# Optimization experiments

Measured on AMD Instinct MI355X. Metric: run time of the kernel, lower is better.

Reference implementation:

```python
import jax, jax.numpy as jnp
import numpy as np

HEAD_SIZE = 128  # hidden_size 2048 / 16 heads; used only as softmax scale in this module


def setup_inputs() -> dict:
    key = jax.random.key(0)
    ks = jax.random.split(key, 4)
    B, S, H = 2, 4096, 2048
    hidden_states = jax.random.normal(ks[0], (B, S, H), dtype=jnp.float32)
    attention_mask = jnp.zeros((B, 1, S), dtype=jnp.float32)  # additive mask, broadcasts onto [B,S,S]
    s = 1.0 / np.sqrt(H)
    Wq = jax.random.normal(ks[1], (H, H), dtype=jnp.float32) * s
    Wk = jax.random.normal(ks[2], (H, H), dtype=jnp.float32) * s
    Wv = jax.random.normal(ks[3], (H, H), dtype=jnp.float32) * s
    bq = jnp.zeros((H,), dtype=jnp.float32)
    bk = jnp.zeros((H,), dtype=jnp.float32)
    bv = jnp.zeros((H,), dtype=jnp.float32)
    return {"hidden_states": hidden_states, "attention_mask": attention_mask,
            "Wq": Wq, "bq": bq, "Wk": Wk, "bk": bk, "Wv": Wv, "bv": bv}


def reference(hidden_states, attention_mask, Wq, bq, Wk, bk, Wv, bv):
    # Self-attention: cross_hidden_states defaults to hidden_states.
    q = jnp.einsum('bsh,oh->bso', hidden_states, Wq) + bq  # [B,S,H]
    k = jnp.einsum('bsh,oh->bso', hidden_states, Wk) + bk
    v = jnp.einsum('bsh,oh->bso', hidden_states, Wv) + bv
    # Note: module never splits heads, so scores are a single [B,S,S] matrix
    scores = jnp.einsum('bqh,bkh->bqk', q, k) / jnp.sqrt(jnp.asarray(HEAD_SIZE, q.dtype))
    scores = scores + attention_mask  # additive mask, broadcast
    probs = jax.nn.softmax(scores, axis=-1)  # dropout p=0 -> identity
    context = jnp.einsum('bqk,bkh->bqh', probs, v)  # [B,S,H]
    return context
```

## Files before the change

### kernel.cpp

```cpp
#include <hip/hip_runtime.h>

typedef _Float16 f16;
typedef _Float16 f16x8 __attribute__((ext_vector_type(8)));
typedef _Float16 f16x4 __attribute__((ext_vector_type(4)));
typedef float    f32x16 __attribute__((ext_vector_type(16)));

#define GLD16(g, l)                                                            \
  __builtin_amdgcn_global_load_lds(                                            \
      (const __attribute__((address_space(1))) void*)(g),                      \
      (__attribute__((address_space(3))) void*)(l), 16, 0, 0)

static constexpr int S = 4096, H = 2048, B = 2;

__global__ __launch_bounds__(256) void cast_all(
    const float* __restrict__ hs, const float* __restrict__ w0,
    const float* __restrict__ w1, const float* __restrict__ w2,
    f16* __restrict__ hs_h, f16* __restrict__ w_h) {
  const int hsN4 = B * S * H / 4;
  const int wN4  = H * H / 4;
  int i = blockIdx.x * 256 + threadIdx.x;
  float4 f;
  if (i < hsN4) {
    f = reinterpret_cast<const float4*>(hs)[i];
    f16x4 h = {(f16)f.x, (f16)f.y, (f16)f.z, (f16)f.w};
    reinterpret_cast<f16x4*>(hs_h)[i] = h;
  } else {
    int j = i - hsN4;
    int seg = j / wN4, off = j - seg * wN4;
    const float* src = seg == 0 ? w0 : (seg == 1 ? w1 : w2);
    f = reinterpret_cast<const float4*>(src)[off];
    f16x4 h = {(f16)f.x, (f16)f.y, (f16)f.z, (f16)f.w};
    reinterpret_cast<f16x4*>(w_h)[j] = h;
  }
}

template <int MODE>
__global__ __launch_bounds__(256) void gemm_tn(
    const f16* __restrict__ A, const f16* __restrict__ Bm,
    void* __restrict__ C0, void* __restrict__ C1, void* __restrict__ C2,
    const float* __restrict__ x0, const float* __restrict__ x1,
    const float* __restrict__ x2, float scale, int K, int lda, int ldb) {
  __shared__ __attribute__((aligned(16))) char smem[32768];
  f16* sA = (f16*)smem;
  f16* sB = (f16*)(smem + 16384);

  const int tileM = blockIdx.y * 128;
  const int tileN = blockIdx.x * 128;

  const int tid  = threadIdx.x;
  const int wave = tid >> 6, lane = tid & 63;
  const int wm = (wave >> 1) * 64, wn = (wave & 1) * 64;
  const int l31 = lane & 31, khalf = lane >> 5;

  f32x16 acc[2][2] = {};

  size_t rowA = tileM, rowB = tileN;
  if (MODE == 2) rowB = (size_t)(tileM >> 12) * S + tileN;
  if (MODE == 3) rowB = (size_t)(tileM >> 12) * H + tileN;
  const f16* gA = A + rowA * lda;
  const f16* gB = Bm + rowB * ldb;

  size_t aoff[4], boff[4];
  int ldsoff[4];
#pragma unroll
  for (int j = 0; j < 4; ++j) {
    int id = j * 256 + tid;
    int r = id >> 3, cs = (id & 7) ^ (r & 7) ^ ((r & 16) >> 2);
    aoff[j] = (size_t)r * lda + cs * 8;
    boff[j] = (size_t)r * ldb + cs * 8;
    ldsoff[j] = id * 8;
  }

  const int rsw = (l31 & 7) ^ ((l31 & 16) >> 2);

  for (int k0 = 0; k0 < K; k0 += 64) {
#pragma unroll
    for (int j = 0; j < 4; ++j) {
      GLD16(gA + aoff[j] + k0, &sA[ldsoff[j]]);
      GLD16(gB + boff[j] + k0, &sB[ldsoff[j]]);
    }
    __syncthreads();
#pragma unroll
    for (int c = 0; c < 4; ++c) {
      f16x8 af[2], bf[2];
      const int pos = ((c * 2 + khalf) ^ rsw) * 8;
#pragma unroll
      for (int x = 0; x < 2; ++x)
        af[x] = *reinterpret_cast<const f16x8*>(&sA[(wm + x * 32 + l31) * 64 + pos]);
#pragma unroll
      for (int y = 0; y < 2; ++y)
        bf[y] = *reinterpret_cast<const f16x8*>(&sB[(wn + y * 32 + l31) * 64 + pos]);
#pragma unroll
      for (int x = 0; x < 2; ++x)
#pragma unroll
        for (int y = 0; y < 2; ++y)
          acc[x][y] = __builtin_amdgcn_mfma_f32_32x32x16_f16(af[x], bf[y], acc[x][y], 0, 0, 0);
    }
    __syncthreads();
  }

  if (MODE == 0 && (tileN >> 11) == 2) {
    const int nn0 = tileN - 2 * H;
    const int b = tileM >> 12, s0 = tileM & (S - 1);
    f16* sT = (f16*)smem;
#pragma unroll
    for (int p = 0; p < 2; ++p) {
      if ((wn >> 6) == p) {
#pragma unroll
        for (int x = 0; x < 2; ++x)
#pragma unroll
          for (int y = 0; y < 2; ++y) {
            int scol = y * 32 + l31;
            float bias = x2[nn0 + p * 64 + scol];
#pragma unroll
            for (int g = 0; g < 4; ++g) {
              int row = wm + x * 32 + g * 8 + khalf * 4;
              f16x4 h4 = {(f16)(acc[x][y][g * 4 + 0] + bias),
                          (f16)(acc[x][y][g * 4 + 1] + bias),
                          (f16)(acc[x][y][g * 4 + 2] + bias),
                          (f16)(acc[x][y][g * 4 + 3] + bias)};
              *reinterpret_cast<f16x4*>(&sT[scol * 136 + row]) = h4;
            }
          }
      }
      __syncthreads();
      {
        int c = tid >> 2, hh = tid & 3;
        const f16* src = &sT[c * 136 + hh * 32];
        f16* dst = (f16*)C2 + (size_t)b * H * S + (size_t)(nn0 + p * 64 + c) * S +
                   s0 + hh * 32;
#pragma unroll
        for (int j = 0; j < 4; ++j)
          reinterpret_cast<f16x8*>(dst)[j] = reinterpret_cast<const f16x8*>(src)[j];
      }
      __syncthreads();
    }
    return;
  }

#pragma unroll
  for (int x = 0; x < 2; ++x)
#pragma unroll
    for (int y = 0; y < 2; ++y)
#pragma unroll
      for (int r = 0; r < 16; ++r) {
        int m = tileM + wm + x * 32 + (r & 3) + 8 * (r >> 2) + 4 * khalf;
        int n = tileN + wn + y * 32 + l31;
        float v = acc[x][y][r];
        if (MODE == 0) {
          int seg = n >> 11, nn = n & 2047;
          if (seg == 0) {
            ((f16*)C0)[(size_t)m * H + nn] = (f16)(v + x0[nn]);
          } else {
            ((f16*)C1)[(size_t)m * H + nn] = (f16)(v + x1[nn]);
          }
        } else if (MODE == 2) {
          int b = m >> 12;
          ((f16*)C0)[(size_t)m * S + n] = (f16)(v * scale + x0[(size_t)b * S + n]);
        } else {
          ((float*)C0)[(size_t)m * H + n] = v;
        }
      }
}

__global__ __launch_bounds__(256) void softmax_f16(f16* __restrict__ sc) {
  const int tid = threadIdx.x;
  f16* rp = sc + (size_t)blockIdx.x * S;
  f16x8 h[2];
#pragma unroll
  for (int j = 0; j < 2; ++j) h[j] = reinterpret_cast<f16x8*>(rp)[tid + j * 256];

  float v[16];
#pragma unroll
  for (int j = 0; j < 2; ++j)
#pragma unroll
    for (int e = 0; e < 8; ++e) v[j * 8 + e] = (float)h[j][e];

  float m = -1e30f;
#pragma unroll
  for (int e = 0; e < 16; ++e) m = fmaxf(m, v[e]);
#pragma unroll
  for (int off = 32; off; off >>= 1) m = fmaxf(m, __shfl_xor(m, off));

  __shared__ float red[8];
  int wave = tid >> 6, lane = tid & 63;
  if (lane == 0) red[wave] = m;
  __syncthreads();
  m = fmaxf(fmaxf(red[0], red[1]), fmaxf(red[2], red[3]));

  float s = 0.f;
#pragma unroll
  for (int e = 0; e < 16; ++e) { v[e] = __expf(v[e] - m); s += v[e]; }
#pragma unroll
  for (int off = 32; off; off >>= 1) s += __shfl_xor(s, off);
  if (lane == 0) red[4 + wave] = s;
  __syncthreads();
  s = red[4] + red[5] + red[6] + red[7];
  float inv = 1.0f / s;

#pragma unroll
  for (int j = 0; j < 2; ++j) {
#pragma unroll
    for (int e = 0; e < 8; ++e) h[j][e] = (f16)(v[j * 8 + e] * inv);
    reinterpret_cast<f16x8*>(rp)[tid + j * 256] = h[j];
  }
}

extern "C" void kernel_launch(void* const* d_in, const int* in_sizes, int n_in,
                              void* d_out, int out_size, void* d_ws, size_t ws_size,
                              hipStream_t stream) {
  const float* hs   = (const float*)d_in[0];
  const float* mask = (const float*)d_in[1];
  const float* Wq   = (const float*)d_in[2];
  const float* bq   = (const float*)d_in[3];
  const float* Wk   = (const float*)d_in[4];
  const float* bk   = (const float*)d_in[5];
  const float* Wv   = (const float*)d_in[6];
  const float* bv   = (const float*)d_in[7];
  float* out = (float*)d_out;

  f16* hs_h = (f16*)d_ws;
  f16* w_h  = hs_h + (size_t)B * S * H;
  f16* Qh   = w_h + (size_t)3 * H * H;
  f16* Kh   = Qh + (size_t)B * S * H;
  f16* Vt   = Kh + (size_t)B * S * H;
  f16* Sc   = Vt + (size_t)B * S * H;

  const int castN = B * S * H / 4 + 3 * H * H / 4;
  cast_all<<<(castN + 255) / 256, 256, 0, stream>>>(hs, Wq, Wk, Wv, hs_h, w_h);

  dim3 blk(256);
  const float sscale = 0.088388347648318447f;

  gemm_tn<0><<<dim3(48, 64), blk, 0, stream>>>(
      hs_h, w_h, Qh, Kh, Vt, bq, bk, bv, 1.f, H, H, H);

  gemm_tn<2><<<dim3(32, 64), blk, 0, stream>>>(
      Qh, Kh, Sc, nullptr, nullptr, mask, nullptr, nullptr, sscale, H, H, H);

  softmax_f16<<<B * S, 256, 0, stream>>>(Sc);

  gemm_tn<3><<<dim3(16, 64), blk, 0, stream>>>(
      Sc, Vt, out, nullptr, nullptr, nullptr, nullptr, nullptr, 1.f, S, S, S);
}
```

Measured before the change: 736.1 us.

## Triple-buffer LDS with async prefetch and 256x128 tiles in GEMM kernel

Rewrites the shared GEMM main loop to use 512-thread blocks with a 256x128 output tile. A three-stage LDS ring buffer is prefetched two k-steps ahead with global_load_lds, and the loads are interleaved between the two half-k MFMA phases using explicit vmcnt waits, raw barriers and s_setprio. The goal is to hide global-load latency behind matrix work and raise reuse of each B tile. In exchange it uses about 147KB of LDS per block, which limits occupancy to one block per CU, and the hand-placed waitcnt and barrier logic is fragile.

Result: no change. 740.3 us (+0.6%).

```diff
diff --git a/kernel.cpp b/kernel.cpp
--- a/kernel.cpp
+++ b/kernel.cpp
@@ -35,68 +35,136 @@
 }
 
 template <int MODE>
-__global__ __launch_bounds__(256) void gemm_tn(
+__global__ __launch_bounds__(512, 2) void gemm_tn(
     const f16* __restrict__ A, const f16* __restrict__ Bm,
     void* __restrict__ C0, void* __restrict__ C1, void* __restrict__ C2,
     const float* __restrict__ x0, const float* __restrict__ x1,
     const float* __restrict__ x2, float scale, int K, int lda, int ldb) {
-  __shared__ __attribute__((aligned(16))) char smem[32768];
-  f16* sA = (f16*)smem;
-  f16* sB = (f16*)(smem + 16384);
-
-  const int tileM = blockIdx.y * 128;
+  __shared__ __attribute__((aligned(16))) char smem[147456];
+
+  const int tileM = blockIdx.y * 256;
   const int tileN = blockIdx.x * 128;
 
   const int tid  = threadIdx.x;
   const int wave = tid >> 6, lane = tid & 63;
-  const int wm = (wave >> 1) * 64, wn = (wave & 1) * 64;
+  const int wm = (wave >> 1) * 64;
+  const int wn = (wave & 1) * 64;
   const int l31 = lane & 31, khalf = lane >> 5;
 
   f32x16 acc[2][2] = {};
 
-  size_t rowA = tileM, rowB = tileN;
+  size_t rowB = tileN;
   if (MODE == 2) rowB = (size_t)(tileM >> 12) * S + tileN;
   if (MODE == 3) rowB = (size_t)(tileM >> 12) * H + tileN;
-  const f16* gA = A + rowA * lda;
+  const f16* gA = A + (size_t)tileM * lda;
   const f16* gB = Bm + rowB * ldb;
 
-  size_t aoff[4], boff[4];
-  int ldsoff[4];
+  int aoff[4], aloff[4], boff[2], bloff[2];
 #pragma unroll
   for (int j = 0; j < 4; ++j) {
-    int id = j * 256 + tid;
+    int id = j * 512 + tid;
     int r = id >> 3, cs = (id & 7) ^ (r & 7) ^ ((r & 16) >> 2);
-    aoff[j] = (size_t)r * lda + cs * 8;
-    boff[j] = (size_t)r * ldb + cs * 8;
-    ldsoff[j] = id * 8;
+    aoff[j]  = r * lda + cs * 8;
+    aloff[j] = id * 8;
+  }
+#pragma unroll
+  for (int j = 0; j < 2; ++j) {
+    int id = j * 512 + tid;
+    int r = id >> 3, cs = (id & 7) ^ (r & 7) ^ ((r & 16) >> 2);
+    boff[j]  = r * ldb + cs * 8;
+    bloff[j] = id * 8;
   }
 
   const int rsw = (l31 & 7) ^ ((l31 & 16) >> 2);
-
-  for (int k0 = 0; k0 < K; k0 += 64) {
-#pragma unroll
-    for (int j = 0; j < 4; ++j) {
-      GLD16(gA + aoff[j] + k0, &sA[ldsoff[j]]);
-      GLD16(gB + boff[j] + k0, &sB[ldsoff[j]]);
-    }
-    __syncthreads();
-#pragma unroll
-    for (int c = 0; c < 4; ++c) {
-      f16x8 af[2], bf[2];
+  const int nt = K >> 6;
+
+  {
+    f16* sA0 = (f16*)smem;
+    f16* sB0 = (f16*)(smem + 32768);
+    f16* sA1 = (f16*)(smem + 49152);
+    f16* sB1 = (f16*)(smem + 49152 + 32768);
+#pragma unroll
+    for (int j = 0; j < 4; ++j) GLD16(gA + aoff[j], &sA0[aloff[j]]);
+#pragma unroll
+    for (int j = 0; j < 2; ++j) GLD16(gB + boff[j], &sB0[bloff[j]]);
+#pragma unroll
+    for (int j = 0; j < 4; ++j) GLD16(gA + aoff[j] + 64, &sA1[aloff[j]]);
+#pragma unroll
+    for (int j = 0; j < 2; ++j) GLD16(gB + boff[j] + 64, &sB1[bloff[j]]);
+  }
+  asm volatile("s_waitcnt vmcnt(6)" ::: "memory");
+  __builtin_amdgcn_s_barrier();
+
+  int cOff = 0, pOff = 2 * 49152;
+  for (int t = 0; t < nt; ++t) {
+    const f16* sA = (const f16*)(smem + cOff);
+    const f16* sB = (const f16*)(smem + cOff + 32768);
+    f16* pA = (f16*)(smem + pOff);
+    f16* pB = (f16*)(smem + pOff + 32768);
+    const int kg = (t + 2) * 64;
+    const bool pf = (t + 2 < nt);
+
+    f16x8 af[2][2], bf[2][2];
+
+#pragma unroll
+    for (int c = 0; c < 2; ++c) {
       const int pos = ((c * 2 + khalf) ^ rsw) * 8;
 #pragma unroll
       for (int x = 0; x < 2; ++x)
-        af[x] = *reinterpret_cast<const f16x8*>(&sA[(wm + x * 32 + l31) * 64 + pos]);
+        af[c][x] = *reinterpret_cast<const f16x8*>(&sA[(wm + x * 32 + l31) * 64 + pos]);
 #pragma unroll
       for (int y = 0; y < 2; ++y)
-        bf[y] = *reinterpret_cast<const f16x8*>(&sB[(wn + y * 32 + l31) * 64 + pos]);
+        bf[c][y] = *reinterpret_cast<const f16x8*>(&sB[(wn + y * 32 + l31) * 64 + pos]);
+    }
+    if (pf) {
+      GLD16(gA + aoff[0] + kg, &pA[aloff[0]]);
+      GLD16(gA + aoff[1] + kg, &pA[aloff[1]]);
+      GLD16(gA + aoff[2] + kg, &pA[aloff[2]]);
+    }
+    __builtin_amdgcn_s_barrier();
+    __builtin_amdgcn_s_setprio(1);
+#pragma unroll
+    for (int c = 0; c < 2; ++c)
 #pragma unroll
       for (int x = 0; x < 2; ++x)
 #pragma unroll
         for (int y = 0; y < 2; ++y)
-          acc[x][y] = __builtin_amdgcn_mfma_f32_32x32x16_f16(af[x], bf[y], acc[x][y], 0, 0, 0);
-    }
-    __syncthreads();
+          acc[x][y] = __builtin_amdgcn_mfma_f32_32x32x16_f16(af[c][x], bf[c][y], acc[x][y], 0, 0, 0);
+    __builtin_amdgcn_s_setprio(0);
+    __builtin_amdgcn_s_barrier();
+
+#pragma unroll
+    for (int c = 0; c < 2; ++c) {
+      const int pos = (((c + 2) * 2 + khalf) ^ rsw) * 8;
+#pragma unroll
+      for (int x = 0; x < 2; ++x)
+        af[c][x] = *reinterpret_cast<const f16x8*>(&sA[(wm + x * 32 + l31) * 64 + pos]);
+#pragma unroll
+      for (int y = 0; y < 2; ++y)
+        bf[c][y] = *reinterpret_cast<const f16x8*>(&sB[(wn + y * 32 + l31) * 64 + pos]);
+    }
+    if (pf) {
+      GLD16(gA + aoff[3] + kg, &pA[aloff[3]]);
+      GLD16(gB + boff[0] + kg, &pB[bloff[0]]);
+      GLD16(gB + boff[1] + kg, &pB[bloff[1]]);
+      asm volatile("s_waitcnt vmcnt(6)" ::: "memory");
+    } else {
+      asm volatile("s_waitcnt vmcnt(0)" ::: "memory");
+    }
+    __builtin_amdgcn_s_barrier();
+    __builtin_amdgcn_s_setprio(1);
+#pragma unroll
+    for (int c = 0; c < 2; ++c)
+#pragma unroll
+      for (int x = 0; x < 2; ++x)
+#pragma unroll
+        for (int y = 0; y < 2; ++y)
+          acc[x][y] = __builtin_amdgcn_mfma_f32_32x32x16_f16(af[c][x], bf[c][y], acc[x][y], 0, 0, 0);
+    __builtin_amdgcn_s_setprio(0);
+    __builtin_amdgcn_s_barrier();
+
+    cOff += 49152; if (cOff == 147456) cOff = 0;
+    pOff += 49152; if (pOff == 147456) pOff = 0;
   }
 
   if (MODE == 0 && (tileN >> 11) == 2) {
@@ -119,14 +187,14 @@
                           (f16)(acc[x][y][g * 4 + 1] + bias),
                           (f16)(acc[x][y][g * 4 + 2] + bias),
                           (f16)(acc[x][y][g * 4 + 3] + bias)};
-              *reinterpret_cast<f16x4*>(&sT[scol * 136 + row]) = h4;
+              *reinterpret_cast<f16x4*>(&sT[scol * 264 + row]) = h4;
             }
           }
       }
       __syncthreads();
       {
-        int c = tid >> 2, hh = tid & 3;
-        const f16* src = &sT[c * 136 + hh * 32];
+        int c = tid >> 3, hh = tid & 7;
+        const f16* src = &sT[c * 264 + hh * 32];
         f16* dst = (f16*)C2 + (size_t)b * H * S + (size_t)(nn0 + p * 64 + c) * S +
                    s0 + hh * 32;
 #pragma unroll
@@ -229,17 +297,17 @@
   const int castN = B * S * H / 4 + 3 * H * H / 4;
   cast_all<<<(castN + 255) / 256, 256, 0, stream>>>(hs, Wq, Wk, Wv, hs_h, w_h);
 
-  dim3 blk(256);
+  dim3 blk(512);
   const float sscale = 0.088388347648318447f;
 
-  gemm_tn<0><<<dim3(48, 64), blk, 0, stream>>>(
+  gemm_tn<0><<<dim3(48, 32), blk, 0, stream>>>(
       hs_h, w_h, Qh, Kh, Vt, bq, bk, bv, 1.f, H, H, H);
 
-  gemm_tn<2><<<dim3(32, 64), blk, 0, stream>>>(
+  gemm_tn<2><<<dim3(32, 32), blk, 0, stream>>>(
       Qh, Kh, Sc, nullptr, nullptr, mask, nullptr, nullptr, sscale, H, H, H);
 
   softmax_f16<<<B * S, 256, 0, stream>>>(Sc);
 
-  gemm_tn<3><<<dim3(16, 64), blk, 0, stream>>>(
+  gemm_tn<3><<<dim3(16, 32), blk, 0, stream>>>(
       Sc, Vt, out, nullptr, nullptr, nullptr, nullptr, nullptr, 1.f, S, S, S);
 }
```

## Use 256x256 tiles with double-buffered LDS prefetch in GEMM kernel

Applied to the files above, without the earlier changes.

The GEMM kernel moves from 128x128 tiles with 256 threads to 256x256 tiles with 512 threads, each wave computing a 128x64 sub-tile. LDS is double-buffered (128 KB) so the next K-slice is prefetched through global_load_lds while MFMAs run on the current one, leaving one barrier per iteration. MFMA sections are wrapped in s_setprio. The intent is better data reuse and overlap of memory with compute, at the cost of much higher LDS use per block, fewer blocks in flight, and grids (256 to 768 blocks) that may fill the 256 CUs unevenly.

New measurement: 659.4 us. 1.12x faster.

```diff
diff --git a/kernel.cpp b/kernel.cpp
--- a/kernel.cpp
+++ b/kernel.cpp
@@ -35,68 +35,88 @@
 }
 
 template <int MODE>
-__global__ __launch_bounds__(256) void gemm_tn(
+__global__ __launch_bounds__(512, 2) void gemm_tn(
     const f16* __restrict__ A, const f16* __restrict__ Bm,
     void* __restrict__ C0, void* __restrict__ C1, void* __restrict__ C2,
     const float* __restrict__ x0, const float* __restrict__ x1,
     const float* __restrict__ x2, float scale, int K, int lda, int ldb) {
-  __shared__ __attribute__((aligned(16))) char smem[32768];
-  f16* sA = (f16*)smem;
-  f16* sB = (f16*)(smem + 16384);
-
-  const int tileM = blockIdx.y * 128;
-  const int tileN = blockIdx.x * 128;
+  __shared__ __attribute__((aligned(16))) char smem[131072];
+
+  const int tileM = blockIdx.y * 256;
+  const int tileN = blockIdx.x * 256;
 
   const int tid  = threadIdx.x;
   const int wave = tid >> 6, lane = tid & 63;
-  const int wm = (wave >> 1) * 64, wn = (wave & 1) * 64;
+  const int wm = (wave >> 2) * 128;
+  const int wn = (wave & 3) * 64;
   const int l31 = lane & 31, khalf = lane >> 5;
 
-  f32x16 acc[2][2] = {};
-
-  size_t rowA = tileM, rowB = tileN;
+  f32x16 acc[4][2] = {};
+
+  size_t rowB = tileN;
   if (MODE == 2) rowB = (size_t)(tileM >> 12) * S + tileN;
   if (MODE == 3) rowB = (size_t)(tileM >> 12) * H + tileN;
-  const f16* gA = A + rowA * lda;
+  const f16* gA = A + (size_t)tileM * lda;
   const f16* gB = Bm + rowB * ldb;
 
-  size_t aoff[4], boff[4];
-  int ldsoff[4];
+  int aoff[4], boff[4], loff[4];
 #pragma unroll
   for (int j = 0; j < 4; ++j) {
-    int id = j * 256 + tid;
+    int id = j * 512 + tid;
     int r = id >> 3, cs = (id & 7) ^ (r & 7) ^ ((r & 16) >> 2);
-    aoff[j] = (size_t)r * lda + cs * 8;
-    boff[j] = (size_t)r * ldb + cs * 8;
-    ldsoff[j] = id * 8;
+    aoff[j] = r * lda + cs * 8;
+    boff[j] = r * ldb + cs * 8;
+    loff[j] = id * 8;
   }
 
   const int rsw = (l31 & 7) ^ ((l31 & 16) >> 2);
-
-  for (int k0 = 0; k0 < K; k0 += 64) {
-#pragma unroll
-    for (int j = 0; j < 4; ++j) {
-      GLD16(gA + aoff[j] + k0, &sA[ldsoff[j]]);
-      GLD16(gB + boff[j] + k0, &sB[ldsoff[j]]);
+  const int nt = K >> 6;
+
+  {
+    f16* pA = (f16*)smem;
+    f16* pB = (f16*)(smem + 32768);
+#pragma unroll
+    for (int j = 0; j < 4; ++j) GLD16(gA + aoff[j], &pA[loff[j]]);
+#pragma unroll
+    for (int j = 0; j < 4; ++j) GLD16(gB + boff[j], &pB[loff[j]]);
+  }
+  asm volatile("s_waitcnt vmcnt(0)" ::: "memory");
+  __builtin_amdgcn_s_barrier();
+
+  for (int t = 0; t < nt; ++t) {
+    const int cur = t & 1;
+    const f16* sA = (const f16*)(smem + cur * 65536);
+    const f16* sB = (const f16*)(smem + cur * 65536 + 32768);
+    const bool pf = (t + 1 < nt);
+    if (pf) {
+      f16* pA = (f16*)(smem + (cur ^ 1) * 65536);
+      f16* pB = (f16*)(smem + (cur ^ 1) * 65536 + 32768);
+      const int kg = (t + 1) * 64;
+#pragma unroll
+      for (int j = 0; j < 4; ++j) GLD16(gA + aoff[j] + kg, &pA[loff[j]]);
+#pragma unroll
+      for (int j = 0; j < 4; ++j) GLD16(gB + boff[j] + kg, &pB[loff[j]]);
     }
-    __syncthreads();
 #pragma unroll
     for (int c = 0; c < 4; ++c) {
-      f16x8 af[2], bf[2];
       const int pos = ((c * 2 + khalf) ^ rsw) * 8;
-#pragma unroll
-      for (int x = 0; x < 2; ++x)
+      f16x8 af[4], bf[2];
+#pragma unroll
+      for (int x = 0; x < 4; ++x)
         af[x] = *reinterpret_cast<const f16x8*>(&sA[(wm + x * 32 + l31) * 64 + pos]);
 #pragma unroll
       for (int y = 0; y < 2; ++y)
         bf[y] = *reinterpret_cast<const f16x8*>(&sB[(wn + y * 32 + l31) * 64 + pos]);
-#pragma unroll
-      for (int x = 0; x < 2; ++x)
+      __builtin_amdgcn_s_setprio(1);
+#pragma unroll
+      for (int x = 0; x < 4; ++x)
 #pragma unroll
         for (int y = 0; y < 2; ++y)
           acc[x][y] = __builtin_amdgcn_mfma_f32_32x32x16_f16(af[x], bf[y], acc[x][y], 0, 0, 0);
+      __builtin_amdgcn_s_setprio(0);
     }
-    __syncthreads();
+    if (pf) asm volatile("s_waitcnt vmcnt(0)" ::: "memory");
+    __builtin_amdgcn_s_barrier();
   }
 
   if (MODE == 0 && (tileN >> 11) == 2) {
@@ -104,10 +124,10 @@
     const int b = tileM >> 12, s0 = tileM & (S - 1);
     f16* sT = (f16*)smem;
 #pragma unroll
-    for (int p = 0; p < 2; ++p) {
-      if ((wn >> 6) == p) {
-#pragma unroll
-        for (int x = 0; x < 2; ++x)
+    for (int p = 0; p < 4; ++p) {
+      if ((wave & 3) == p) {
+#pragma unroll
+        for (int x = 0; x < 4; ++x)
 #pragma unroll
           for (int y = 0; y < 2; ++y) {
             int scol = y * 32 + l31;
@@ -119,14 +139,14 @@
                           (f16)(acc[x][y][g * 4 + 1] + bias),
                           (f16)(acc[x][y][g * 4 + 2] + bias),
                           (f16)(acc[x][y][g * 4 + 3] + bias)};
-              *reinterpret_cast<f16x4*>(&sT[scol * 136 + row]) = h4;
+              *reinterpret_cast<f16x4*>(&sT[scol * 264 + row]) = h4;
             }
           }
       }
       __syncthreads();
       {
-        int c = tid >> 2, hh = tid & 3;
-        const f16* src = &sT[c * 136 + hh * 32];
+        int c = tid >> 3, hh = tid & 7;
+        const f16* src = &sT[c * 264 + hh * 32];
         f16* dst = (f16*)C2 + (size_t)b * H * S + (size_t)(nn0 + p * 64 + c) * S +
                    s0 + hh * 32;
 #pragma unroll
@@ -139,7 +159,7 @@
   }
 
 #pragma unroll
-  for (int x = 0; x < 2; ++x)
+  for (int x = 0; x < 4; ++x)
 #pragma unroll
     for (int y = 0; y < 2; ++y)
 #pragma unroll
@@ -229,17 +249,17 @@
   const int castN = B * S * H / 4 + 3 * H * H / 4;
   cast_all<<<(castN + 255) / 256, 256, 0, stream>>>(hs, Wq, Wk, Wv, hs_h, w_h);
 
-  dim3 blk(256);
+  dim3 blk(512);
   const float sscale = 0.088388347648318447f;
 
-  gemm_tn<0><<<dim3(48, 64), blk, 0, stream>>>(
+  gemm_tn<0><<<dim3(24, 32), blk, 0, stream>>>(
       hs_h, w_h, Qh, Kh, Vt, bq, bk, bv, 1.f, H, H, H);
 
-  gemm_tn<2><<<dim3(32, 64), blk, 0, stream>>>(
+  gemm_tn<2><<<dim3(16, 32), blk, 0, stream>>>(
       Qh, Kh, Sc, nullptr, nullptr, mask, nullptr, nullptr, sscale, H, H, H);
 
   softmax_f16<<<B * S, 256, 0, stream>>>(Sc);
 
-  gemm_tn<3><<<dim3(16, 64), blk, 0, stream>>>(
+  gemm_tn<3><<<dim3(8, 32), blk, 0, stream>>>(
       Sc, Vt, out, nullptr, nullptr, nullptr, nullptr, nullptr, 1.f, S, S, S);
 }
```
